# Kernel optimization log

Hardware: AMD Instinct MI355X
Metric: run time of the kernel (lower is better)

The kernel has to match this reference:

```python
import jax, jax.numpy as jnp
import numpy as np

N_NODES = 100000
N_EDGES = 3200000
N_GRAPHS = 1024
D = 64
STEPS_PROP = 6
STEPS_S2S = 6


def setup_inputs() -> dict:
    key = jax.random.key(0)
    ks = jax.random.split(key, 16)
    inp = {}
    inp['x'] = jax.random.normal(ks[0], (N_NODES, 15), dtype=jnp.float32)
    inp['edge_index'] = jax.random.randint(ks[1], (2, N_EDGES), 0, N_NODES, dtype=jnp.int64 if jax.config.jax_enable_x64 else jnp.int32)
    inp['batch'] = jnp.sort(jax.random.randint(ks[2], (N_NODES,), 0, N_GRAPHS, dtype=jnp.int64 if jax.config.jax_enable_x64 else jnp.int32))
    s = 0.1
    inp['W0'] = jax.random.normal(ks[3], (15, D), dtype=jnp.float32) * s
    inp['b0'] = jax.random.normal(ks[4], (D,), dtype=jnp.float32) * s
    inp['Wc'] = jax.random.normal(ks[5], (D, D), dtype=jnp.float32) * s
    inp['bc'] = jax.random.normal(ks[6], (D,), dtype=jnp.float32) * s
    inp['Wih'] = jax.random.normal(ks[7], (4 * D, 2 * D), dtype=jnp.float32) * s
    inp['Whh'] = jax.random.normal(ks[8], (4 * D, D), dtype=jnp.float32) * s
    inp['bih'] = jax.random.normal(ks[9], (4 * D,), dtype=jnp.float32) * s
    inp['bhh'] = jax.random.normal(ks[10], (4 * D,), dtype=jnp.float32) * s
    inp['W1'] = jax.random.normal(ks[11], (2 * D, D), dtype=jnp.float32) * s
    inp['b1'] = jax.random.normal(ks[12], (D,), dtype=jnp.float32) * s
    inp['W2'] = jax.random.normal(ks[13], (D, 12), dtype=jnp.float32) * s
    inp['b2'] = jax.random.normal(ks[14], (12,), dtype=jnp.float32) * s
    return inp


def _gcn_forward(x, edge_index, batch, W0, b0, Wc, bc, Wih, Whh, bih, bhh, W1, b1, W2, b2):
    N = x.shape[0]
    # GCNConv normalization with self-loops (PyG semantics): A_hat = D^-1/2 (A+I) D^-1/2
    loops = jnp.arange(N, dtype=edge_index.dtype)
    row = jnp.concatenate([edge_index[0], loops])  # source
    col = jnp.concatenate([edge_index[1], loops])  # target
    deg = jax.ops.segment_sum(jnp.ones_like(col, dtype=x.dtype), col, num_segments=N)
    dinv = jnp.where(deg > 0, jax.lax.rsqrt(jnp.maximum(deg, 1e-30)), 0.0)
    norm = dinv[row] * dinv[col]  # [E+N]

    out = jax.nn.relu(x @ W0 + b0)  # [N, D]
    for _ in range(STEPS_PROP):
        h = out @ Wc  # transform first
        msg = h[row] * norm[:, None]  # gather along edges
        out = jax.nn.relu(jax.ops.segment_sum(msg, col, num_segments=N) + bc)

    # Set2Set pooling
    B = N_GRAPHS
    d = out.shape[1]
    h_l = jnp.zeros((B, d), dtype=out.dtype)
    c_l = jnp.zeros((B, d), dtype=out.dtype)
    q_star = jnp.zeros((B, 2 * d), dtype=out.dtype)
    for _ in range(STEPS_S2S):
        gates = q_star @ Wih.T + h_l @ Whh.T + bih + bhh  # [B, 4d]
        i_g, f_g, g_g, o_g = jnp.split(gates, 4, axis=1)
        c_l = jax.nn.sigmoid(f_g) * c_l + jax.nn.sigmoid(i_g) * jnp.tanh(g_g)
        h_l = jax.nn.sigmoid(o_g) * jnp.tanh(c_l)
        q = h_l  # [B, d]
        e = jnp.sum(out * q[batch], axis=-1)  # [N]
        m = jax.ops.segment_max(e, batch, num_segments=B)
        a_num = jnp.exp(e - m[batch])
        denom = jax.ops.segment_sum(a_num, batch, num_segments=B)
        a = a_num / denom[batch]
        r = jax.ops.segment_sum(a[:, None] * out, batch, num_segments=B)  # [B, d]
        q_star = jnp.concatenate([q, r], axis=-1)

    y = jax.nn.relu(q_star @ W1 + b1)
    return y @ W2 + b2  # [B, 12]


def reference(x, edge_index, batch, W0, b0, Wc, bc, Wih, Whh, bih, bhh, W1, b1, W2, b2):
    return _gcn_forward(x, edge_index, batch, W0, b0, Wc, bc, Wih, Whh, bih, bhh, W1, b1, W2, b2)
```

## Files before the change

### kernel.cpp

```cpp
#include <hip/hip_runtime.h>
#include <hip/hip_fp16.h>
#include <math.h>

#define ND 64
constexpr int BKT_SHIFT = 9;
constexpr int BKT_MASK = (1 << BKT_SHIFT) - 1;
constexpr int BCUR_PAD = 16;
constexpr int STG_TILE = 8192;

__device__ __forceinline__ float sigmoidf_(float x){ return 1.f/(1.f+__expf(-x)); }
__device__ __forceinline__ __half2 h2lo(uint2 v){ return *reinterpret_cast<__half2*>(&v.x); }
__device__ __forceinline__ __half2 h2hi(uint2 v){ return *reinterpret_cast<__half2*>(&v.y); }
__device__ __forceinline__ __half2 shxor_h2(__half2 h, int off){
  unsigned u = *reinterpret_cast<unsigned*>(&h);
  u = __shfl_xor(u, off, 64);
  return *reinterpret_cast<__half2*>(&u);
}

__global__ void k_bhist(const int* __restrict__ col, int* __restrict__ bgcnt,
                        int E, int NBK){
  __shared__ int lhist[512];
  int t0 = blockIdx.x * STG_TILE;
  int t1 = t0 + STG_TILE; if (t1 > E) t1 = E;
  for (int i = threadIdx.x; i < NBK; i += 256) lhist[i] = 0;
  __syncthreads();
  for (int i = t0 + threadIdx.x; i < t1; i += 256)
    atomicAdd(&lhist[col[i] >> BKT_SHIFT], 1);
  __syncthreads();
  for (int i = threadIdx.x; i < NBK; i += 256)
    if (lhist[i] > 0) atomicAdd(&bgcnt[i], lhist[i]);
}

__global__ void k_bscan(const int* __restrict__ bgcnt, int* __restrict__ bstart,
                        int* __restrict__ rowptr, int NBK, int E, int N){
  __shared__ int tmp[256];
  int t = threadIdx.x;
  int v = (t < NBK) ? bgcnt[t] : 0;
  tmp[t] = v; __syncthreads();
  for (int off=1; off<256; off<<=1){
    int u = (t>=off) ? tmp[t-off] : 0;
    __syncthreads();
    tmp[t] += u;
    __syncthreads();
  }
  if (t <= NBK) bstart[t] = (t==0) ? 0 : tmp[t-1];
  if (t == 0) rowptr[N] = E;
}

__global__ void k_bcinit(const int* __restrict__ bstart, int* __restrict__ bcur, int NBK){
  int b = blockIdx.x*blockDim.x + threadIdx.x;
  if (b < NBK) bcur[b*BCUR_PAD] = bstart[b];
}

__global__ void k_stage2(const int* __restrict__ row, const int* __restrict__ col,
                         int* __restrict__ bcur, unsigned* __restrict__ pairs,
                         int E, int NBK){
  __shared__ int lhist[512];
  __shared__ int lbase[512];
  int t0 = blockIdx.x * STG_TILE;
  int t1 = t0 + STG_TILE; if (t1 > E) t1 = E;
  for (int i = threadIdx.x; i < NBK; i += 256) lhist[i] = 0;
  __syncthreads();
  for (int i = t0 + threadIdx.x; i < t1; i += 256)
    atomicAdd(&lhist[col[i] >> BKT_SHIFT], 1);
  __syncthreads();
  for (int i = threadIdx.x; i < NBK; i += 256){
    int c = lhist[i];
    lbase[i] = (c > 0) ? atomicAdd(&bcur[i*BCUR_PAD], c) : 0;
    lhist[i] = 0;
  }
  __syncthreads();
  for (int i = t0 + threadIdx.x; i < t1; i += 256){
    int d = col[i];
    int b = d >> BKT_SHIFT;
    int pos = lbase[b] + atomicAdd(&lhist[b], 1);
    pairs[pos] = ((unsigned)row[i] << BKT_SHIFT) | (unsigned)(d & BKT_MASK);
  }
}

__global__ void k_place(const unsigned* __restrict__ pairs, const int* __restrict__ bstart,
                        int* __restrict__ rowptr, float* __restrict__ dinv,
                        int* __restrict__ csr, int N){
  __shared__ int h[1 << BKT_SHIFT];
  __shared__ int excl[1 << BKT_SHIFT];
  __shared__ int tsum[256];
  int b = blockIdx.x;
  int base = b << BKT_SHIFT;
  int nend = base + (1 << BKT_SHIFT); if (nend > N) nend = N;
  int cnt = nend - base;
  int t = threadIdx.x;
  int s = bstart[b], e = bstart[b+1];

  h[2*t] = 0; h[2*t+1] = 0;
  __syncthreads();
  for (int i = s + t; i < e; i += 256)
    atomicAdd(&h[pairs[i] & BKT_MASK], 1);
  __syncthreads();
  int a0 = h[2*t], a1 = h[2*t+1];
  tsum[t] = a0 + a1;
  __syncthreads();
  for (int off=1; off<256; off<<=1){
    int u = (t>=off) ? tsum[t-off] : 0;
    __syncthreads();
    tsum[t] += u;
    __syncthreads();
  }
  int base0 = (t==0) ? 0 : tsum[t-1];
  excl[2*t]   = base0;
  excl[2*t+1] = base0 + a0;
  __syncthreads();
  for (int c = t; c < cnt; c += 256){
    int deg = h[c];
    rowptr[base + c] = s + excl[c];
    dinv[base + c] = rsqrtf((float)(deg + 1));
  }
  __syncthreads();
  for (int c = t; c < cnt; c += 256) h[c] = s + excl[c];
  __syncthreads();
  for (int i = s + t; i < e; i += 256){
    unsigned p = pairs[i];
    int pos = atomicAdd(&h[p & BKT_MASK], 1);
    csr[pos] = (int)(p >> BKT_SHIFT);
  }
}

__global__ void k_input(const float* __restrict__ x, const float* __restrict__ W0,
                        const float* __restrict__ b0, const float* __restrict__ dinv,
                        __half* __restrict__ s, int N){
  __shared__ float w0s[15*ND];
  __shared__ float b0s[ND];
  int tid = threadIdx.x;
  for (int i=tid; i<15*ND; i+=256) w0s[i] = W0[i];
  if (tid < ND) b0s[tid] = b0[tid];
  __syncthreads();
  int node = blockIdx.x*4 + (tid>>6);
  int f = tid & 63;
  if (node < N){
    float acc = b0s[f];
    const float* xr = x + (size_t)node*15;
    #pragma unroll
    for (int k=0;k<15;k++) acc += xr[k]*w0s[k*ND+f];
    s[(size_t)node*ND+f] = __float2half_rn(dinv[node]*fmaxf(acc, 0.f));
  }
}

__global__ void k_prop(const __half* __restrict__ sbuf, const int* __restrict__ rowptr,
                       const int* __restrict__ csr, const float* __restrict__ dinv,
                       const float* __restrict__ Wc, const float* __restrict__ bc,
                       __half* __restrict__ s_new, __half* __restrict__ outh,
                       int N, int wout){
  __shared__ float wcs[ND*ND];
  __shared__ float xs[16][ND];
  __shared__ float bcs[ND];
  const uint2* g8 = (const uint2*)sbuf;
  int tid = threadIdx.x;
  for (int i=tid; i<ND*ND; i+=256) wcs[i] = Wc[i];
  if (tid < ND) bcs[tid] = bc[tid];
  int nb = blockIdx.x*16;
  int wv = tid>>6, lane = tid&63;
  int grp = lane>>4, li = lane&15;

  for (int q=0; q<4; ++q){
    int node = nb + wv*4 + q;
    float val = 0.f;
    if (node < N){
      int s = rowptr[node], e = rowptr[node+1];
      __half2 z = __float2half2_rn(0.f);
      __half2 a0x=z,a0y=z, a1x=z,a1y=z, a2x=z,a2y=z, a3x=z,a3y=z;
      int i = s;
      for (; i + 16 <= e; i += 16){
        int s0 = csr[i +  0 + grp];
        int s1 = csr[i +  4 + grp];
        int s2 = csr[i +  8 + grp];
        int s3 = csr[i + 12 + grp];
        uint2 v0 = g8[(size_t)s0*16 + li];
        uint2 v1 = g8[(size_t)s1*16 + li];
        uint2 v2 = g8[(size_t)s2*16 + li];
        uint2 v3 = g8[(size_t)s3*16 + li];
        a0x = __hadd2(a0x, h2lo(v0)); a0y = __hadd2(a0y, h2hi(v0));
        a1x = __hadd2(a1x, h2lo(v1)); a1y = __hadd2(a1y, h2hi(v1));
        a2x = __hadd2(a2x, h2lo(v2)); a2y = __hadd2(a2y, h2hi(v2));
        a3x = __hadd2(a3x, h2lo(v3)); a3y = __hadd2(a3y, h2hi(v3));
      }
      for (; i + 4 <= e; i += 4){
        int s0 = csr[i + grp];
        uint2 v0 = g8[(size_t)s0*16 + li];
        a0x = __hadd2(a0x, h2lo(v0)); a0y = __hadd2(a0y, h2hi(v0));
      }
      int r = e - i;
      if (grp < r){
        int s0 = csr[i + grp];
        uint2 v0 = g8[(size_t)s0*16 + li];
        a1x = __hadd2(a1x, h2lo(v0)); a1y = __hadd2(a1y, h2hi(v0));
      }
      __half2 sxh = __hadd2(__hadd2(a0x,a1x), __hadd2(a2x,a3x));
      __half2 syh = __hadd2(__hadd2(a0y,a1y), __hadd2(a2y,a3y));
      sxh = __hadd2(sxh, shxor_h2(sxh, 16));
      syh = __hadd2(syh, shxor_h2(syh, 16));
      sxh = __hadd2(sxh, shxor_h2(sxh, 32));
      syh = __hadd2(syh, shxor_h2(syh, 32));
      uint2 sv = g8[(size_t)node*16 + li];
      sxh = __hadd2(sxh, h2lo(sv));
      syh = __hadd2(syh, h2hi(sv));
      val = (grp==0) ? __half2float(__low2half(sxh))
          : (grp==1) ? __half2float(__high2half(sxh))
          : (grp==2) ? __half2float(__low2half(syh))
          :            __half2float(__high2half(syh));
    }
    xs[wv*4+q][4*li+grp] = val;
  }
  __syncthreads();

  int f = tid&63, nq = tid>>6;
  float acc0=0.f, acc1=0.f, acc2=0.f, acc3=0.f;
  #pragma unroll 16
  for (int k=0;k<ND;k++){
    float w = wcs[k*ND+f];
    acc0 += w*xs[nq*4+0][k];
    acc1 += w*xs[nq*4+1][k];
    acc2 += w*xs[nq*4+2][k];
    acc3 += w*xs[nq*4+3][k];
  }
  int n0 = nb + nq*4;
  float bcf = bcs[f];
  #pragma unroll
  for (int j=0; j<4; ++j){
    int node = n0 + j;
    if (node < N){
      float a = (j==0)?acc0:(j==1)?acc1:(j==2)?acc2:acc3;
      float dn = dinv[node];
      float r = fmaxf(dn*a + bcf, 0.f);
      if (wout) outh[(size_t)node*ND+f] = __float2half_rn(r);
      else      s_new[(size_t)node*ND+f] = __float2half_rn(dn*r);
    }
  }
}

__global__ void k_goff(const int* __restrict__ batch, int* __restrict__ goff, int N, int B){
  int i = blockIdx.x*blockDim.x + threadIdx.x;
  if (i >= N) return;
  int b = batch[i];
  if (i == 0){ for (int g2=0; g2<=b; ++g2) goff[g2]=0; }
  else {
    int bp = batch[i-1];
    for (int g2=bp+1; g2<=b; ++g2) goff[g2]=i;
  }
  if (i == N-1){ for (int g2=b+1; g2<=B; ++g2) goff[g2]=N; }
}

__global__ void k_s2s(const __half* __restrict__ nodef, const int* __restrict__ goff,
                      const float* __restrict__ Wih, const float* __restrict__ Whh,
                      const float* __restrict__ bih, const float* __restrict__ bhh,
                      const float* __restrict__ W1, const float* __restrict__ b1,
                      const float* __restrict__ W2, const float* __restrict__ b2,
                      float* __restrict__ outy, int B){
  __shared__ float qsr[2][128];
  __shared__ float hlr[2][64];
  __shared__ float clr[2][64];
  __shared__ float gat[2][256];
  __shared__ float redm[2][2], redd[2][2];
  __shared__ float redr[2][2][64];
  __shared__ float yy[2][64];
  int tid = threadIdx.x;
  int g0 = blockIdx.x*2;
  if (g0 >= B) return;
  for (int i=tid;i<2*128;i+=256) qsr[i>>7][i&127]=0.f;
  if (tid<128){ hlr[tid>>6][tid&63]=0.f; clr[tid>>6][tid&63]=0.f; }
  __syncthreads();
  int lane=tid&63, wv=tid>>6;
  int gg_w = wv>>1, wp = wv&1;
  for (int step=0; step<6; ++step){
    float bb = bih[tid]+bhh[tid];
    float a0=bb, a1=bb;
    const float* wr = Wih + (size_t)tid*128;
    for (int k=0;k<128;k++){ float w=wr[k]; a0+=w*qsr[0][k]; a1+=w*qsr[1][k]; }
    const float* wr2 = Whh + (size_t)tid*64;
    for (int k=0;k<64;k++){ float w=wr2[k]; a0+=w*hlr[0][k]; a1+=w*hlr[1][k]; }
    gat[0][tid]=a0; gat[1][tid]=a1;
    __syncthreads();
    if (tid<128){
      int gg=tid>>6, d=tid&63;
      float ig=sigmoidf_(gat[gg][d]);
      float fg=sigmoidf_(gat[gg][64+d]);
      float gv=tanhf(gat[gg][128+d]);
      float og=sigmoidf_(gat[gg][192+d]);
      float c = fg*clr[gg][d]+ig*gv;
      float h = og*tanhf(c);
      clr[gg][d]=c; hlr[gg][d]=h; qsr[gg][d]=h;
    }
    __syncthreads();
    {
      int g = g0+gg_w;
      int s = goff[g], e = goff[g+1];
      float q = hlr[gg_w][lane];
      float m=-3.0e38f, denom=0.f, racc=0.f;
      for (int n=s+wp; n<e; n+=2){
        float v = __half2float(nodef[(size_t)n*64+lane]);
        float p = v*q;
        #pragma unroll
        for (int off=32; off>=1; off>>=1) p += __shfl_xor(p, off, 64);
        if (p>m){ float sc=__expf(m-p); denom*=sc; racc*=sc; m=p; }
        float w=__expf(p-m);
        denom+=w; racc+=w*v;
      }
      if (lane==0){ redm[gg_w][wp]=m; redd[gg_w][wp]=denom; }
      redr[gg_w][wp][lane]=racc;
    }
    __syncthreads();
    if (wp==0){
      float m0=redm[gg_w][0], m1=redm[gg_w][1];
      float mm=fmaxf(m0,m1);
      float s0=__expf(m0-mm), s1=__expf(m1-mm);
      float dt=redd[gg_w][0]*s0+redd[gg_w][1]*s1;
      float rs=redr[gg_w][0][lane]*s0+redr[gg_w][1][lane]*s1;
      qsr[gg_w][64+lane] = (dt>0.f)? rs/dt : 0.f;
    }
    __syncthreads();
  }
  if (tid<128){
    int gg=tid>>6, f=tid&63;
    float acc=b1[f];
    for (int k=0;k<128;k++) acc += qsr[gg][k]*W1[k*64+f];
    yy[gg][f]=fmaxf(acc,0.f);
  }
  __syncthreads();
  if (tid<24){
    int gg=tid/12, o=tid%12;
    float a2=b2[o];
    for (int k=0;k<64;k++) a2 += yy[gg][k]*W2[k*12+o];
    outy[(size_t)(g0+gg)*12+o]=a2;
  }
}

extern "C" void kernel_launch(void* const* d_in, const int* in_sizes, int n_in,
                              void* d_out, int out_size, void* d_ws, size_t ws_size,
                              hipStream_t stream){
  const float* x    = (const float*)d_in[0];
  const int*   ei   = (const int*)d_in[1];
  const int*   batch= (const int*)d_in[2];
  const float* W0   = (const float*)d_in[3];
  const float* b0   = (const float*)d_in[4];
  const float* Wc   = (const float*)d_in[5];
  const float* bc   = (const float*)d_in[6];
  const float* Wih  = (const float*)d_in[7];
  const float* Whh  = (const float*)d_in[8];
  const float* bih  = (const float*)d_in[9];
  const float* bhh  = (const float*)d_in[10];
  const float* W1   = (const float*)d_in[11];
  const float* b1   = (const float*)d_in[12];
  const float* W2   = (const float*)d_in[13];
  const float* b2   = (const float*)d_in[14];
  float* yout = (float*)d_out;

  const int N = in_sizes[0]/15;
  const int E = in_sizes[1]/2;
  const int B = out_size/12;
  const int NBK = (N + (1<<BKT_SHIFT) - 1) >> BKT_SHIFT;
  const int* row = ei;
  const int* col = ei + E;

  char* ws = (char*)d_ws;
  size_t off = 0;
  auto alloc = [&](size_t bytes)->void*{
    void* p = ws + off; off = (off + bytes + 255) & ~(size_t)255; return p;
  };
  int*      bgcnt   = (int*)     alloc((size_t)(NBK+1)*4);
  int*      bstart  = (int*)     alloc((size_t)(NBK+1)*4);
  int*      bcur    = (int*)     alloc((size_t)NBK*BCUR_PAD*4);
  int*      rowptr  = (int*)     alloc((size_t)(N+1)*4);
  unsigned* pairs   = (unsigned*)alloc((size_t)E*4);
  int*      csr     = (int*)     alloc((size_t)E*4);
  float*    dinv    = (float*)   alloc((size_t)N*4);
  __half*   nodef   = (__half*)  alloc((size_t)N*ND*2);
  __half*   s_a     = (__half*)  alloc((size_t)N*ND*2);
  __half*   s_b     = (__half*)  alloc((size_t)N*ND*2);
  int*      goff    = (int*)     alloc((size_t)(B+1)*4);
  (void)ws_size; (void)n_in;

  hipMemsetAsync(bgcnt, 0, (size_t)(NBK+1)*4, stream);

  int nstg = (E + STG_TILE - 1)/STG_TILE;
  k_bhist <<<nstg, 256, 0, stream>>>(col, bgcnt, E, NBK);
  k_bscan <<<1, 256, 0, stream>>>(bgcnt, bstart, rowptr, NBK, E, N);
  k_bcinit<<<(NBK+255)/256, 256, 0, stream>>>(bstart, bcur, NBK);
  k_stage2<<<nstg, 256, 0, stream>>>(row, col, bcur, pairs, E, NBK);
  k_place <<<NBK, 256, 0, stream>>>(pairs, bstart, rowptr, dinv, csr, N);

  k_input<<<(N+3)/4, 256, 0, stream>>>(x, W0, b0, dinv, s_a, N);
  __half* scur = s_a; __half* snxt = s_b;
  for (int s6=0; s6<6; ++s6){
    k_prop<<<(N+15)/16, 256, 0, stream>>>(scur, rowptr, csr, dinv,
                                          Wc, bc, snxt, nodef, N, (s6==5)?1:0);
    __half* t = scur; scur = snxt; snxt = t;
  }

  k_goff<<<(N+255)/256, 256, 0, stream>>>(batch, goff, N, B);
  k_s2s<<<(B+1)/2, 256, 0, stream>>>(nodef, goff, Wih, Whh, bih, bhh,
                                     W1, b1, W2, b2, yout, B);
}
```

Baseline: 937.7 us.

## Restructure Set2Set kernel: one graph per block, fused LSTM weights, 16-way node split

Set2Set now runs one graph per block (1024 blocks instead of 512), with 16 quarter-wave groups each reading 4 halves per lane via uint2 loads and merging online-softmax partials. A prep kernel transposes the LSTM weights and pre-adds Wih and Whh for the h-dependent half, using the fact that q equals h_l, which halves the gate matvec. Weight reads become coalesced across threads. The cost is an extra small launch and a 16-way reduction per step.

```diff
diff --git a/kernel.cpp b/kernel.cpp
--- a/kernel.cpp
+++ b/kernel.cpp
@@ -248,87 +248,116 @@
   if (i == N-1){ for (int g2=b+1; g2<=B; ++g2) goff[g2]=N; }
 }
 
+__global__ void k_wprep(const float* __restrict__ Wih, const float* __restrict__ Whh,
+                        const float* __restrict__ bih, const float* __restrict__ bhh,
+                        float* __restrict__ WcombT, float* __restrict__ WrT,
+                        float* __restrict__ bsum){
+  int k = blockIdx.x;
+  int j = threadIdx.x;
+  WcombT[k*256 + j] = Wih[(size_t)j*128 + k] + Whh[(size_t)j*64 + k];
+  WrT  [k*256 + j] = Wih[(size_t)j*128 + 64 + k];
+  if (k == 0) bsum[j] = bih[j] + bhh[j];
+}
+
 __global__ void k_s2s(const __half* __restrict__ nodef, const int* __restrict__ goff,
-                      const float* __restrict__ Wih, const float* __restrict__ Whh,
-                      const float* __restrict__ bih, const float* __restrict__ bhh,
+                      const float* __restrict__ WcombT, const float* __restrict__ WrT,
+                      const float* __restrict__ bsum,
                       const float* __restrict__ W1, const float* __restrict__ b1,
                       const float* __restrict__ W2, const float* __restrict__ b2,
                       float* __restrict__ outy, int B){
-  __shared__ float qsr[2][128];
-  __shared__ float hlr[2][64];
-  __shared__ float clr[2][64];
-  __shared__ float gat[2][256];
-  __shared__ float redm[2][2], redd[2][2];
-  __shared__ float redr[2][2][64];
-  __shared__ float yy[2][64];
+  __shared__ float qsr[128];
+  __shared__ float clr[64];
+  __shared__ float gat[256];
+  __shared__ float redm[16], redd[16];
+  __shared__ float redr[16][64];
+  __shared__ float yy[64];
   int tid = threadIdx.x;
-  int g0 = blockIdx.x*2;
-  if (g0 >= B) return;
-  for (int i=tid;i<2*128;i+=256) qsr[i>>7][i&127]=0.f;
-  if (tid<128){ hlr[tid>>6][tid&63]=0.f; clr[tid>>6][tid&63]=0.f; }
-  __syncthreads();
-  int lane=tid&63, wv=tid>>6;
-  int gg_w = wv>>1, wp = wv&1;
+  int g = blockIdx.x;
+  if (g >= B) return;
+  if (tid < 128) qsr[tid] = 0.f;
+  if (tid < 64)  clr[tid] = 0.f;
+  __syncthreads();
+  int lane = tid&63, wv = tid>>6;
+  int grp = lane>>4, li = lane&15;
+  int gidx = wv*4 + grp;
+  int s = goff[g], e = goff[g+1];
+  const uint2* nf = (const uint2*)nodef;
+
   for (int step=0; step<6; ++step){
-    float bb = bih[tid]+bhh[tid];
-    float a0=bb, a1=bb;
-    const float* wr = Wih + (size_t)tid*128;
-    for (int k=0;k<128;k++){ float w=wr[k]; a0+=w*qsr[0][k]; a1+=w*qsr[1][k]; }
-    const float* wr2 = Whh + (size_t)tid*64;
-    for (int k=0;k<64;k++){ float w=wr2[k]; a0+=w*hlr[0][k]; a1+=w*hlr[1][k]; }
-    gat[0][tid]=a0; gat[1][tid]=a1;
-    __syncthreads();
-    if (tid<128){
-      int gg=tid>>6, d=tid&63;
-      float ig=sigmoidf_(gat[gg][d]);
-      float fg=sigmoidf_(gat[gg][64+d]);
-      float gv=tanhf(gat[gg][128+d]);
-      float og=sigmoidf_(gat[gg][192+d]);
-      float c = fg*clr[gg][d]+ig*gv;
+    {
+      float a0 = bsum[tid], a1 = 0.f;
+      for (int k=0; k<64; k+=2){
+        a0 += WcombT[(k  )*256+tid]*qsr[k  ] + WrT[(k  )*256+tid]*qsr[64+k  ];
+        a1 += WcombT[(k+1)*256+tid]*qsr[k+1] + WrT[(k+1)*256+tid]*qsr[64+k+1];
+      }
+      gat[tid] = a0 + a1;
+    }
+    __syncthreads();
+    if (tid < 64){
+      float ig = sigmoidf_(gat[tid]);
+      float fg = sigmoidf_(gat[64+tid]);
+      float gv = tanhf(gat[128+tid]);
+      float og = sigmoidf_(gat[192+tid]);
+      float c = fg*clr[tid] + ig*gv;
       float h = og*tanhf(c);
-      clr[gg][d]=c; hlr[gg][d]=h; qsr[gg][d]=h;
+      clr[tid] = c;
+      qsr[tid] = h;
     }
     __syncthreads();
     {
-      int g = g0+gg_w;
-      int s = goff[g], e = goff[g+1];
-      float q = hlr[gg_w][lane];
-      float m=-3.0e38f, denom=0.f, racc=0.f;
-      for (int n=s+wp; n<e; n+=2){
-        float v = __half2float(nodef[(size_t)n*64+lane]);
-        float p = v*q;
-        #pragma unroll
-        for (int off=32; off>=1; off>>=1) p += __shfl_xor(p, off, 64);
-        if (p>m){ float sc=__expf(m-p); denom*=sc; racc*=sc; m=p; }
-        float w=__expf(p-m);
-        denom+=w; racc+=w*v;
-      }
-      if (lane==0){ redm[gg_w][wp]=m; redd[gg_w][wp]=denom; }
-      redr[gg_w][wp][lane]=racc;
-    }
-    __syncthreads();
-    if (wp==0){
-      float m0=redm[gg_w][0], m1=redm[gg_w][1];
-      float mm=fmaxf(m0,m1);
-      float s0=__expf(m0-mm), s1=__expf(m1-mm);
-      float dt=redd[gg_w][0]*s0+redd[gg_w][1]*s1;
-      float rs=redr[gg_w][0][lane]*s0+redr[gg_w][1][lane]*s1;
-      qsr[gg_w][64+lane] = (dt>0.f)? rs/dt : 0.f;
-    }
-    __syncthreads();
-  }
-  if (tid<128){
-    int gg=tid>>6, f=tid&63;
-    float acc=b1[f];
-    for (int k=0;k<128;k++) acc += qsr[gg][k]*W1[k*64+f];
-    yy[gg][f]=fmaxf(acc,0.f);
-  }
-  __syncthreads();
-  if (tid<24){
-    int gg=tid/12, o=tid%12;
-    float a2=b2[o];
-    for (int k=0;k<64;k++) a2 += yy[gg][k]*W2[k*12+o];
-    outy[(size_t)(g0+gg)*12+o]=a2;
+      float4 q4 = *(const float4*)&qsr[4*li];
+      float m = -3.0e38f, denom = 0.f;
+      float r0=0.f, r1=0.f, r2=0.f, r3=0.f;
+      for (int n = s + gidx; n < e; n += 16){
+        uint2 v = nf[(size_t)n*16 + li];
+        float2 flo = __half22float2(h2lo(v));
+        float2 fhi = __half22float2(h2hi(v));
+        float p = flo.x*q4.x + flo.y*q4.y + fhi.x*q4.z + fhi.y*q4.w;
+        p += __shfl_xor(p, 1, 64);
+        p += __shfl_xor(p, 2, 64);
+        p += __shfl_xor(p, 4, 64);
+        p += __shfl_xor(p, 8, 64);
+        if (p > m){
+          float sc = __expf(m - p);
+          denom *= sc; r0 *= sc; r1 *= sc; r2 *= sc; r3 *= sc;
+          m = p;
+        }
+        float w = __expf(p - m);
+        denom += w;
+        r0 += w*flo.x; r1 += w*flo.y; r2 += w*fhi.x; r3 += w*fhi.y;
+      }
+      if (li == 0){ redm[gidx] = m; redd[gidx] = denom; }
+      redr[gidx][4*li+0] = r0;
+      redr[gidx][4*li+1] = r1;
+      redr[gidx][4*li+2] = r2;
+      redr[gidx][4*li+3] = r3;
+    }
+    __syncthreads();
+    if (tid < 64){
+      float mm = -3.0e38f;
+      #pragma unroll
+      for (int k=0;k<16;k++) mm = fmaxf(mm, redm[k]);
+      float dt = 0.f, rs = 0.f;
+      #pragma unroll
+      for (int k=0;k<16;k++){
+        float sc = __expf(redm[k] - mm);
+        dt += redd[k]*sc;
+        rs += redr[k][tid]*sc;
+      }
+      qsr[64+tid] = (dt > 0.f) ? rs/dt : 0.f;
+    }
+    __syncthreads();
+  }
+  if (tid < 64){
+    float acc = b1[tid];
+    for (int k=0;k<128;k++) acc += qsr[k]*W1[k*64+tid];
+    yy[tid] = fmaxf(acc, 0.f);
+  }
+  __syncthreads();
+  if (tid < 12){
+    float a2 = b2[tid];
+    for (int k=0;k<64;k++) a2 += yy[k]*W2[k*12+tid];
+    outy[(size_t)g*12+tid] = a2;
   }
 }
 
@@ -375,6 +404,9 @@
   __half*   s_a     = (__half*)  alloc((size_t)N*ND*2);
   __half*   s_b     = (__half*)  alloc((size_t)N*ND*2);
   int*      goff    = (int*)     alloc((size_t)(B+1)*4);
+  float*    WcombT  = (float*)   alloc(64*256*4);
+  float*    WrT     = (float*)   alloc(64*256*4);
+  float*    bsum    = (float*)   alloc(256*4);
   (void)ws_size; (void)n_in;
 
   hipMemsetAsync(bgcnt, 0, (size_t)(NBK+1)*4, stream);
@@ -395,6 +427,7 @@
   }
 
   k_goff<<<(N+255)/256, 256, 0, stream>>>(batch, goff, N, B);
-  k_s2s<<<(B+1)/2, 256, 0, stream>>>(nodef, goff, Wih, Whh, bih, bhh,
-                                     W1, b1, W2, b2, yout, B);
-}
+  k_wprep<<<64, 256, 0, stream>>>(Wih, Whh, bih, bhh, WcombT, WrT, bsum);
+  k_s2s<<<B, 256, 0, stream>>>(nodef, goff, WcombT, WrT, bsum,
+                               W1, b1, W2, b2, yout, B);
+}
```

Result: faster. 868.5 us (-7.4%).
